# Kernel tuning notes

Hardware: AMD Instinct MI355X
Metric: run time of the kernel (lower is better)

Reference implementation:

```python
import jax, jax.numpy as jnp
import numpy as np

N = 20000      # nodes
L = 64         # seq_length
E = 64         # emb_size
V = 30000      # vocab_size
HG = 128       # gnn_hidden_size
HT = 128       # text_hidden_size
NE = 640000    # edges
EPS = 1e-12


def _normalize(x):
    # F.normalize(x, p=2, dim=1) on [N, E, L]
    n = jnp.sqrt(jnp.sum(x * x, axis=1, keepdims=True))
    return x / jnp.maximum(n, EPS)


def gcn_conv(x, W, b, src_idx, dst_idx, n_nodes):
    # PyG GCNConv: add self-loops, symmetric normalization D^-1/2 (A+I) D^-1/2 (X W) + b
    h = x @ W                                            # [N, out]
    deg = jnp.zeros((n_nodes,), h.dtype).at[dst_idx].add(1.0) + 1.0  # incl. self-loop
    dinv = jax.lax.rsqrt(deg)
    norm = dinv[src_idx] * dinv[dst_idx]                 # [NE]
    msg = h[src_idx] * norm[:, None]                     # gather + scale
    out = jnp.zeros_like(h).at[dst_idx].add(msg)         # scatter-add to targets
    out = out + h * (dinv * dinv)[:, None]               # self-loop term
    return out + b


def setup_inputs() -> dict:
    key = jax.random.key(0)
    ks = jax.random.split(key, 12)
    rn = lambda k, shape: jax.random.normal(k, shape, jnp.float32) * 0.02
    return {
        "src": jax.random.randint(ks[0], (N, L), 0, V),
        "seg": jax.random.randint(ks[1], (N, L), 0, 3),
        "edge_index": jax.random.randint(ks[2], (2, NE), 0, N),
        "src_emb": rn(ks[3], (V, E)),
        "seg_emb": rn(ks[4], (3, E)),
        "w": jnp.ones((L,), jnp.float32),
        "Wq1": rn(ks[5], (E, HT)), "bq1": jnp.zeros((HT,), jnp.float32),
        "Wq2": rn(ks[6], (HT, E)), "bq2": jnp.zeros((E,), jnp.float32),
        "Wg1": rn(ks[7], (E, HG)), "bg1": jnp.zeros((HG,), jnp.float32),
        "Wg2": rn(ks[8], (HG, E)), "bg2": jnp.zeros((E,), jnp.float32),
        "Wl": rn(ks[9], (E, E)),   "bl": jnp.zeros((E,), jnp.float32),
    }


def reference(src, seg, edge_index, src_emb, seg_emb, w, Wq1, bq1, Wq2, bq2,
              Wg1, bg1, Wg2, bg2, Wl, bl):
    # --- LiteratureEmbedding ---
    se = src_emb[src]                 # [N, L, E]
    ge = seg_emb[seg]                 # [N, L, E]
    sv = se.reshape(-1, E, L)         # raw view (matches torch .view, not transpose)
    gv = ge.reshape(-1, E, L)
    f = (_normalize(w * sv) + _normalize(gv)).sum(-1)   # [N, E]
    # --- query MLP ---
    x = jax.nn.relu(f @ Wq1 + bq1) @ Wq2 + bq2
    # --- two GCN layers ---
    si, di = edge_index[0], edge_index[1]
    x = jax.nn.relu(gcn_conv(x, Wg1, bg1, si, di, N))
    x = jax.nn.relu(gcn_conv(x, Wg2, bg2, si, di, N))
    # --- output linear (dropout is identity in eval) ---
    return x @ Wl + bl
```

## Files before the change

### kernel.cpp

```cpp
#include <hip/hip_runtime.h>

#if defined(__has_builtin)
#if __has_builtin(__builtin_amdgcn_readlane)
#define READLANE(v, l) __builtin_amdgcn_readlane((v), (l))
#else
#define READLANE(v, l) __shfl((v), (l))
#endif
#else
#define READLANE(v, l) __shfl((v), (l))
#endif
__device__ __forceinline__ float readlane_f(float v, int l) {
    return __uint_as_float(READLANE(__float_as_uint(v), l));
}

__device__ __forceinline__ unsigned short f2bf(float x) {
    unsigned u = __float_as_uint(x);
    u += 0x7FFFu + ((u >> 16) & 1u);
    return (unsigned short)(u >> 16);
}

#define CAPLOG 8

__global__ __launch_bounds__(256) void prep0_k(
    const float* __restrict__ src_emb, unsigned short* __restrict__ sbf, int ve,
    const int* __restrict__ si, const int* __restrict__ di,
    int* __restrict__ cursor, int* __restrict__ edge_off, int ne, int eB)
{
    const int b = blockIdx.x, t = threadIdx.x;
    if (b < eB) {
        int i = b * 256 + t;
        if (i < ne) {
            int d = di[i];
            int pos = atomicAdd(cursor + d, 1);
            edge_off[((long)d << CAPLOG) + pos] = si[i] << 7;
        }
        return;
    }
    int i = ((b - eB) * 256 + t) * 4;
    if (i + 3 < ve) {
        float4 v = *(const float4*)&src_emb[i];
        ushort4 u;
        u.x = f2bf(v.x); u.y = f2bf(v.y); u.z = f2bf(v.z); u.w = f2bf(v.w);
        *(ushort4*)&sbf[i] = u;
    } else {
        for (; i < ve; ++i) sbf[i] = f2bf(src_emb[i]);
    }
}

__global__ __launch_bounds__(256) void prep1_k(
    const int* __restrict__ src, const int* __restrict__ seg,
    const unsigned short* __restrict__ sbf, const float* __restrict__ seg_emb,
    const float* __restrict__ wvec, float* __restrict__ f, int nN)
{
    __shared__ float scr[4][16 * 66];
    const int t = threadIdx.x;
    const int wid = t >> 6, q = t & 63;
    const long n = (long)blockIdx.x * 4 + wid;
    if (n >= nN) return;
    const int grp = q >> 4, c = q & 15;

    const int off = src[n * 64 + q] << 7;
    const int sg  = seg[n * 64 + q];
    const float e0 = seg_emb[q], e1 = seg_emb[64 + q], e2 = seg_emb[128 + q];
    const char* base = (const char*)sbf;

    uint2 dreg[16];
    #pragma unroll
    for (int i = 0; i < 16; ++i) {
        int ro = __shfl(off, i * 4 + grp);
        dreg[i] = *(const uint2*)(base + (ro + c * 8));
    }

    float t0 = 0.f, t1 = 0.f, t2 = 0.f, t3 = 0.f;
    #pragma unroll
    for (int i = 0; i < 16; ++i) {
        float v0 = __uint_as_float(dreg[i].x << 16);
        float v1 = __uint_as_float(dreg[i].x & 0xFFFF0000u);
        float v2 = __uint_as_float(dreg[i].y << 16);
        float v3 = __uint_as_float(dreg[i].y & 0xFFFF0000u);
        t0 += v0 * v0; t1 += v1 * v1; t2 += v2 * v2; t3 += v3 * v3;
    }
    t0 += __shfl_xor(t0, 16); t0 += __shfl_xor(t0, 32);
    t1 += __shfl_xor(t1, 16); t1 += __shfl_xor(t1, 32);
    t2 += __shfl_xor(t2, 16); t2 += __shfl_xor(t2, 32);
    t3 += __shfl_xor(t3, 16); t3 += __shfl_xor(t3, 32);

    const float4 wv = *(const float4*)&wvec[c * 4];
    float4 cf;
    cf.x = wv.x / fmaxf(fabsf(wv.x) * sqrtf(t0), 1e-12f);
    cf.y = wv.y / fmaxf(fabsf(wv.y) * sqrtf(t1), 1e-12f);
    cf.z = wv.z / fmaxf(fabsf(wv.z) * sqrtf(t2), 1e-12f);
    cf.w = wv.w / fmaxf(fabsf(wv.w) * sqrtf(t3), 1e-12f);

    unsigned long long b0 = __ballot(sg == 0);
    unsigned long long b1 = __ballot(sg == 1);
    float n0 = (float)__popcll(b0), n1 = (float)__popcll(b1);
    float n2 = 64.f - n0 - n1;
    float g2 = n0 * e0 * e0 + n1 * e1 * e1 + n2 * e2 * e2;
    float rg = 1.f / fmaxf(sqrtf(g2), 1e-12f);
    float p0 = e0 * rg, p1 = e1 * rg, p2 = e2 * rg;
    #pragma unroll
    for (int m = 1; m < 64; m <<= 1) {
        p0 += __shfl_xor(p0, m);
        p1 += __shfl_xor(p1, m);
        p2 += __shfl_xor(p2, m);
    }

    float* sw = scr[wid];
    #pragma unroll
    for (int i = 0; i < 16; ++i) {
        float po = __uint_as_float(dreg[i].x << 16)          * cf.x
                 + __uint_as_float(dreg[i].x & 0xFFFF0000u)  * cf.y
                 + __uint_as_float(dreg[i].y << 16)          * cf.z
                 + __uint_as_float(dreg[i].y & 0xFFFF0000u)  * cf.w;
        sw[c * 66 + i * 4 + grp] = po;
    }
    float out = 0.f;
    #pragma unroll
    for (int c2 = 0; c2 < 16; ++c2)
        out += sw[c2 * 66 + q];

    const float dg = (sg == 0) ? p0 : ((sg == 1) ? p1 : p2);
    f[n * 64 + q] = out + dg;
}

__device__ __forceinline__ float4 csr_gather4_bf(const char* __restrict__ hb,
                                                 const int* __restrict__ eo,
                                                 int dn, int j, int zoff)
{
    const int grp = j >> 4;
    const int col = (j & 15) << 3;
    float4 a0 = make_float4(0.f, 0.f, 0.f, 0.f);
    float4 a1 = a0, a2 = a0, a3 = a0;
#define ACC(d, a)                                                        \
    { a.x += __uint_as_float((d).x << 16);                               \
      a.y += __uint_as_float((d).x & 0xFFFF0000u);                       \
      a.z += __uint_as_float((d).y << 16);                               \
      a.w += __uint_as_float((d).y & 0xFFFF0000u); }
    for (int e = 0; e < dn; e += 64) {
        const int cnt = min(dn - e, 64);
        const int eoff = (e + j < dn) ? eo[e + j] : zoff;
        int m = 0;
        for (; m + 16 <= cnt; m += 16) {
            int o0 = __shfl(eoff, m + grp);
            int o1 = __shfl(eoff, m + 4 + grp);
            int o2 = __shfl(eoff, m + 8 + grp);
            int o3 = __shfl(eoff, m + 12 + grp);
            uint2 d0 = *(const uint2*)(hb + (o0 + col));
            uint2 d1 = *(const uint2*)(hb + (o1 + col));
            uint2 d2 = *(const uint2*)(hb + (o2 + col));
            uint2 d3 = *(const uint2*)(hb + (o3 + col));
            ACC(d0, a0); ACC(d1, a1); ACC(d2, a2); ACC(d3, a3);
        }
        for (; m < cnt; m += 4) {
            int o = __shfl(eoff, m + grp);
            uint2 d = *(const uint2*)(hb + (o + col));
            ACC(d, a0);
        }
    }
#undef ACC
    a0.x += a1.x + a2.x + a3.x;
    a0.y += a1.y + a2.y + a3.y;
    a0.z += a1.z + a2.z + a3.z;
    a0.w += a1.w + a2.w + a3.w;
    a0.x += __shfl_xor(a0.x, 16); a0.x += __shfl_xor(a0.x, 32);
    a0.y += __shfl_xor(a0.y, 16); a0.y += __shfl_xor(a0.y, 32);
    a0.z += __shfl_xor(a0.z, 16); a0.z += __shfl_xor(a0.z, 32);
    a0.w += __shfl_xor(a0.w, 16); a0.w += __shfl_xor(a0.w, 32);
    return a0;
}

__device__ __forceinline__ float4 bf_row4(const char* hb, long rowoff, int col) {
    uint2 d = *(const uint2*)(hb + rowoff + col);
    float4 v;
    v.x = __uint_as_float(d.x << 16);
    v.y = __uint_as_float(d.x & 0xFFFF0000u);
    v.z = __uint_as_float(d.y << 16);
    v.w = __uint_as_float(d.y & 0xFFFF0000u);
    return v;
}

template <bool S2_BIAS>
__device__ __forceinline__ void dense_pair_body(
    float* Wh, float* F, float* H,
    const float* __restrict__ W1, const float* __restrict__ b1,
    const float* __restrict__ W2, const float* __restrict__ b2,
    const int* __restrict__ deg, unsigned short* __restrict__ out,
    int row0, int nrows, int t)
{
    for (int i = t * 4; i < 32 * 128; i += 1024)
        *(float4*)&Wh[i] = *(const float4*)&W1[i];
    __syncthreads();

    const int jg = t & 31, rslot = t >> 5;
    const int j0 = jg * 4;
    float4 acc0, acc1;
    {
        float4 b4 = *(const float4*)&b1[j0];
        acc0 = b4; acc1 = b4;
    }
    #pragma unroll 2
    for (int k = 0; k < 32; k += 4) {
        float4 w0 = *(float4*)&Wh[(k + 0) * 128 + j0];
        float4 w1 = *(float4*)&Wh[(k + 1) * 128 + j0];
        float4 w2 = *(float4*)&Wh[(k + 2) * 128 + j0];
        float4 w3 = *(float4*)&Wh[(k + 3) * 128 + j0];
        float4 fa = *(float4*)&F[rslot * 64 + k];
        float4 fb = *(float4*)&F[(rslot + 8) * 64 + k];
        acc0.x += fa.x * w0.x + fa.y * w1.x + fa.z * w2.x + fa.w * w3.x;
        acc0.y += fa.x * w0.y + fa.y * w1.y + fa.z * w2.y + fa.w * w3.y;
        acc0.z += fa.x * w0.z + fa.y * w1.z + fa.z * w2.z + fa.w * w3.z;
        acc0.w += fa.x * w0.w + fa.y * w1.w + fa.z * w2.w + fa.w * w3.w;
        acc1.x += fb.x * w0.x + fb.y * w1.x + fb.z * w2.x + fb.w * w3.x;
        acc1.y += fb.x * w0.y + fb.y * w1.y + fb.z * w2.y + fb.w * w3.y;
        acc1.z += fb.x * w0.z + fb.y * w1.z + fb.z * w2.z + fb.w * w3.z;
        acc1.w += fb.x * w0.w + fb.y * w1.w + fb.z * w2.w + fb.w * w3.w;
    }
    __syncthreads();
    for (int i = t * 4; i < 32 * 128; i += 1024)
        *(float4*)&Wh[i] = *(const float4*)&W1[32 * 128 + i];
    __syncthreads();
    #pragma unroll 2
    for (int k = 0; k < 32; k += 4) {
        float4 w0 = *(float4*)&Wh[(k + 0) * 128 + j0];
        float4 w1 = *(float4*)&Wh[(k + 1) * 128 + j0];
        float4 w2 = *(float4*)&Wh[(k + 2) * 128 + j0];
        float4 w3 = *(float4*)&Wh[(k + 3) * 128 + j0];
        float4 fa = *(float4*)&F[rslot * 64 + 32 + k];
        float4 fb = *(float4*)&F[(rslot + 8) * 64 + 32 + k];
        acc0.x += fa.x * w0.x + fa.y * w1.x + fa.z * w2.x + fa.w * w3.x;
        acc0.y += fa.x * w0.y + fa.y * w1.y + fa.z * w2.y + fa.w * w3.y;
        acc0.z += fa.x * w0.z + fa.y * w1.z + fa.z * w2.z + fa.w * w3.z;
        acc0.w += fa.x * w0.w + fa.y * w1.w + fa.z * w2.w + fa.w * w3.w;
        acc1.x += fb.x * w0.x + fb.y * w1.x + fb.z * w2.x + fb.w * w3.x;
        acc1.y += fb.x * w0.y + fb.y * w1.y + fb.z * w2.y + fb.w * w3.y;
        acc1.z += fb.x * w0.z + fb.y * w1.z + fb.z * w2.z + fb.w * w3.z;
        acc1.w += fb.x * w0.w + fb.y * w1.w + fb.z * w2.w + fb.w * w3.w;
    }
    {
        float4 v;
        v.x = fmaxf(acc0.x, 0.f); v.y = fmaxf(acc0.y, 0.f);
        v.z = fmaxf(acc0.z, 0.f); v.w = fmaxf(acc0.w, 0.f);
        *(float4*)&H[rslot * 128 + j0] = v;
        v.x = fmaxf(acc1.x, 0.f); v.y = fmaxf(acc1.y, 0.f);
        v.z = fmaxf(acc1.z, 0.f); v.w = fmaxf(acc1.w, 0.f);
        *(float4*)&H[(rslot + 8) * 128 + j0] = v;
    }
    __syncthreads();

    for (int i = t * 4; i < 64 * 64; i += 1024)
        *(float4*)&Wh[i] = *(const float4*)&W2[i];
    __syncthreads();
    const int jg2 = t & 15, r2 = t >> 4;
    const int j02 = jg2 * 4;
    float4 acc = S2_BIAS ? *(const float4*)&b2[j02]
                         : make_float4(0.f, 0.f, 0.f, 0.f);
    #pragma unroll 2
    for (int k = 0; k < 64; k += 4) {
        float4 w0 = *(float4*)&Wh[(k + 0) * 64 + j02];
        float4 w1 = *(float4*)&Wh[(k + 1) * 64 + j02];
        float4 w2 = *(float4*)&Wh[(k + 2) * 64 + j02];
        float4 w3 = *(float4*)&Wh[(k + 3) * 64 + j02];
        float4 fq = *(float4*)&H[r2 * 128 + k];
        acc.x += fq.x * w0.x + fq.y * w1.x + fq.z * w2.x + fq.w * w3.x;
        acc.y += fq.x * w0.y + fq.y * w1.y + fq.z * w2.y + fq.w * w3.y;
        acc.z += fq.x * w0.z + fq.y * w1.z + fq.z * w2.z + fq.w * w3.z;
        acc.w += fq.x * w0.w + fq.y * w1.w + fq.z * w2.w + fq.w * w3.w;
    }
    __syncthreads();
    for (int i = t * 4; i < 64 * 64; i += 1024)
        *(float4*)&Wh[i] = *(const float4*)&W2[64 * 64 + i];
    __syncthreads();
    #pragma unroll 2
    for (int k = 0; k < 64; k += 4) {
        float4 w0 = *(float4*)&Wh[(k + 0) * 64 + j02];
        float4 w1 = *(float4*)&Wh[(k + 1) * 64 + j02];
        float4 w2 = *(float4*)&Wh[(k + 2) * 64 + j02];
        float4 w3 = *(float4*)&Wh[(k + 3) * 64 + j02];
        float4 fq = *(float4*)&H[r2 * 128 + 64 + k];
        acc.x += fq.x * w0.x + fq.y * w1.x + fq.z * w2.x + fq.w * w3.x;
        acc.y += fq.x * w0.y + fq.y * w1.y + fq.z * w2.y + fq.w * w3.y;
        acc.z += fq.x * w0.z + fq.y * w1.z + fq.z * w2.z + fq.w * w3.z;
        acc.w += fq.x * w0.w + fq.y * w1.w + fq.z * w2.w + fq.w * w3.w;
    }
    const int r = row0 + r2;
    if (r < nrows) {
        float sc = rsqrtf((float)deg[r] + 1.0f);
        ushort4 v;
        v.x = f2bf(acc.x * sc); v.y = f2bf(acc.y * sc);
        v.z = f2bf(acc.z * sc); v.w = f2bf(acc.w * sc);
        *(ushort4*)&out[(long)r * 64 + j02] = v;
    }
}

template <bool S2_BIAS>
__global__ __launch_bounds__(256, 5) void fused2_k(
    const float* __restrict__ in, const float* __restrict__ W1,
    const float* __restrict__ b1, const float* __restrict__ W2,
    const float* __restrict__ b2, const int* __restrict__ deg,
    unsigned short* __restrict__ out, int nrows)
{
    __shared__ __align__(16) float Wh[32 * 128];
    __shared__ __align__(16) float F[16 * 64];
    __shared__ __align__(16) float H[16 * 128];
    const int t = threadIdx.x;
    const int row0 = blockIdx.x * 16;

    for (int i = t * 4; i < 16 * 64; i += 1024) {
        int r = i >> 6;
        float4 v = make_float4(0.f, 0.f, 0.f, 0.f);
        if (row0 + r < nrows) v = *(const float4*)&in[(long)row0 * 64 + i];
        *(float4*)&F[i] = v;
    }
    dense_pair_body<S2_BIAS>(Wh, F, H, W1, b1, W2, b2, deg, out, row0, nrows, t);
}

__global__ __launch_bounds__(256, 5) void gcnfused_k(
    const unsigned short* __restrict__ C, const int* __restrict__ deg,
    const int* __restrict__ edge_off,
    const float* __restrict__ W1, const float* __restrict__ b1,
    const float* __restrict__ W2, unsigned short* __restrict__ out,
    int nrows, int zoff)
{
    __shared__ __align__(16) float Wh[32 * 128];
    __shared__ __align__(16) float F[16 * 64];
    __shared__ __align__(16) float H[16 * 128];
    const int t = threadIdx.x;
    const int row0 = blockIdx.x * 16;
    const int wv = t >> 6, j = t & 63;
    const int col = (j & 15) << 3;

    const char* hb = (const char*)C;
    #pragma unroll
    for (int i = 0; i < 4; ++i) {
        const int r = wv * 4 + i;
        const int node = row0 + r;
        if (node < nrows) {
            float4 agg = csr_gather4_bf(hb, edge_off + ((long)node << CAPLOG),
                                        deg[node], j, zoff);
            float4 self = bf_row4(hb, (long)node << 7, col);
            float dv = rsqrtf((float)deg[node] + 1.0f);
            if ((j >> 4) == 0) {
                float4 res;
                res.x = dv * (self.x + agg.x);
                res.y = dv * (self.y + agg.y);
                res.z = dv * (self.z + agg.z);
                res.w = dv * (self.w + agg.w);
                *(float4*)&F[r * 64 + (j & 15) * 4] = res;
            }
        } else if ((j >> 4) == 0) {
            *(float4*)&F[r * 64 + (j & 15) * 4] = make_float4(0.f, 0.f, 0.f, 0.f);
        }
    }
    dense_pair_body<false>(Wh, F, H, W1, b1, W2, nullptr, deg, out, row0, nrows, t);
}

__global__ __launch_bounds__(256) void gatherout_k(
    const unsigned short* __restrict__ hp, const int* __restrict__ deg,
    const int* __restrict__ edge_off,
    const float* __restrict__ bg2, const float* __restrict__ Wl,
    const float* __restrict__ bl, float* __restrict__ out, int n, int zoff)
{
    __shared__ __align__(16) float WlL[64 * 64];
    __shared__ __align__(16) float vS[4][64];
    const int t = threadIdx.x;
    for (int i = t * 4; i < 64 * 64; i += 1024)
        *(float4*)&WlL[i] = *(const float4*)&Wl[i];
    __syncthreads();

    const int row0 = blockIdx.x * 16;
    const int wv = t >> 6, j = t & 63;
    const int col = (j & 15) << 3;
    const char* hb = (const char*)hp;
    const float blj = bl[j];
    const float4 bg4 = *(const float4*)&bg2[(j & 15) * 4];

    #pragma unroll
    for (int i = 0; i < 4; ++i) {
        const int node = row0 + wv * 4 + i;
        if (node >= n) continue;
        float4 agg = csr_gather4_bf(hb, edge_off + ((long)node << CAPLOG),
                                    deg[node], j, zoff);
        float4 self = bf_row4(hb, (long)node << 7, col);
        const float dv = rsqrtf((float)deg[node] + 1.0f);
        float4 vf;
        vf.x = fmaxf(dv * (self.x + agg.x) + bg4.x, 0.f);
        vf.y = fmaxf(dv * (self.y + agg.y) + bg4.y, 0.f);
        vf.z = fmaxf(dv * (self.z + agg.z) + bg4.z, 0.f);
        vf.w = fmaxf(dv * (self.w + agg.w) + bg4.w, 0.f);
        if ((j >> 4) == 0) *(float4*)&vS[wv][(j & 15) * 4] = vf;
        const float v = vS[wv][j];

        float o = blj;
        #pragma unroll 4
        for (int k = 0; k < 64; k += 4) {
            float vk0 = readlane_f(v, k + 0);
            float vk1 = readlane_f(v, k + 1);
            float vk2 = readlane_f(v, k + 2);
            float vk3 = readlane_f(v, k + 3);
            o += vk0 * WlL[(k + 0) * 64 + j] + vk1 * WlL[(k + 1) * 64 + j]
               + vk2 * WlL[(k + 2) * 64 + j] + vk3 * WlL[(k + 3) * 64 + j];
        }
        out[(long)node * 64 + j] = o;
    }
}

extern "C" void kernel_launch(void* const* d_in, const int* in_sizes, int n_in,
                              void* d_out, int out_size, void* d_ws, size_t ws_size,
                              hipStream_t stream) {
    const int*   src     = (const int*)  d_in[0];
    const int*   seg     = (const int*)  d_in[1];
    const int*   ei      = (const int*)  d_in[2];
    const float* src_emb = (const float*)d_in[3];
    const float* seg_emb = (const float*)d_in[4];
    const float* w       = (const float*)d_in[5];
    const float* Wq1     = (const float*)d_in[6];
    const float* bq1     = (const float*)d_in[7];
    const float* Wq2     = (const float*)d_in[8];
    const float* bq2     = (const float*)d_in[9];
    const float* Wg1     = (const float*)d_in[10];
    const float* bg1     = (const float*)d_in[11];
    const float* Wg2     = (const float*)d_in[12];
    const float* bg2     = (const float*)d_in[13];
    const float* Wl      = (const float*)d_in[14];
    const float* bl      = (const float*)d_in[15];
    float* out = (float*)d_out;

    const int N  = in_sizes[0] / 64;
    const int NE = in_sizes[2] / 2;
    const int VE = in_sizes[3];
    const int* si = ei;
    const int* di = ei + NE;

    const size_t Npad  = ((size_t)N + 3) & ~(size_t)3;
    const size_t VEpad = ((size_t)VE + 7) & ~(size_t)7;
    int* cursor   = (int*)d_ws;
    int* edge_off = cursor + Npad;
    unsigned short* sbf = (unsigned short*)(edge_off + ((size_t)N << CAPLOG));
    float* A32 = (float*)(sbf + VEpad);
    unsigned short* Cbf = (unsigned short*)(A32 + (size_t)N * 64);
    unsigned short* Abf = Cbf + (size_t)N * 64 + 64;
    const int zoff = N << 7;

    dim3 b256(256);
    const int convB = (VE + 1023) / 1024;
    const int eB    = (NE + 255) / 256;
    const int nB    = (N + 3) / 4;
    const int fB    = (N + 15) / 16;

    hipMemsetAsync(cursor, 0, Npad * sizeof(int), stream);
    hipMemsetAsync(Cbf + (size_t)N * 64, 0, 128, stream);
    hipMemsetAsync(Abf + (size_t)N * 64, 0, 128, stream);

    prep0_k<<<eB + convB, b256, 0, stream>>>(src_emb, sbf, VE,
                                             si, di, cursor, edge_off, NE, eB);

    prep1_k<<<nB, b256, 0, stream>>>(src, seg, sbf, seg_emb, w, A32, N);

    fused2_k<true><<<fB, b256, 0, stream>>>(A32, Wq1, bq1, Wq2, bq2,
                                            cursor, Cbf, N);

    gcnfused_k<<<fB, b256, 0, stream>>>(Cbf, cursor, edge_off,
                                        Wg1, bg1, Wg2, Abf, N, zoff);

    gatherout_k<<<fB, b256, 0, stream>>>(Abf, cursor, edge_off, bg2,
                                         Wl, bl, out, N, zoff);
}
```

Measured before the change: 221.8 us.

## Replace fixed-capacity per-node edge buckets with compact CSR built via prefix scan

Edges are now bucketed in two passes. A degree count runs first, then a single-block exclusive scan builds row pointers, and a second atomic pass places source offsets into a compact CSR array. The placement pass is merged into the embedding kernel launch. This replaces the padded 256-slot-per-node layout, shrinking the workspace, making gather index reads contiguous, and removing the hard degree cap. In exchange it adds a serial single-block scan launch and a second pass over the edge list with atomics.

```diff
diff --git a/kernel.cpp b/kernel.cpp
--- a/kernel.cpp
+++ b/kernel.cpp
@@ -19,21 +19,14 @@
     return (unsigned short)(u >> 16);
 }
 
-#define CAPLOG 8
-
 __global__ __launch_bounds__(256) void prep0_k(
     const float* __restrict__ src_emb, unsigned short* __restrict__ sbf, int ve,
-    const int* __restrict__ si, const int* __restrict__ di,
-    int* __restrict__ cursor, int* __restrict__ edge_off, int ne, int eB)
+    const int* __restrict__ di, int* __restrict__ cursor, int ne, int eB)
 {
     const int b = blockIdx.x, t = threadIdx.x;
     if (b < eB) {
         int i = b * 256 + t;
-        if (i < ne) {
-            int d = di[i];
-            int pos = atomicAdd(cursor + d, 1);
-            edge_off[((long)d << CAPLOG) + pos] = si[i] << 7;
-        }
+        if (i < ne) atomicAdd(cursor + di[i], 1);
         return;
     }
     int i = ((b - eB) * 256 + t) * 4;
@@ -47,15 +40,73 @@
     }
 }
 
-__global__ __launch_bounds__(256) void prep1_k(
+__global__ __launch_bounds__(1024) void scan_k(
+    const int* __restrict__ deg, int* __restrict__ rowptr,
+    int* __restrict__ pcur, int n,
+    unsigned* __restrict__ Cz, unsigned* __restrict__ Az)
+{
+    __shared__ int wsum[16];
+    const int t = threadIdx.x;
+    const int lane = t & 63, wid = t >> 6;
+    const int CH = (n + 1023) >> 10;
+    const int base = t * CH;
+
+    int s = 0;
+    for (int i = 0; i < CH; ++i) {
+        int idx = base + i;
+        s += (idx < n) ? deg[idx] : 0;
+    }
+    int x = s;
+    #pragma unroll
+    for (int d = 1; d < 64; d <<= 1) {
+        int v = __shfl_up(x, d);
+        if (lane >= d) x += v;
+    }
+    if (lane == 63) wsum[wid] = x;
+    __syncthreads();
+    if (wid == 0 && lane < 16) {
+        int v = wsum[lane];
+        int y = v;
+        #pragma unroll
+        for (int d = 1; d < 16; d <<= 1) {
+            int u = __shfl_up(y, d);
+            if (lane >= d) y += u;
+        }
+        wsum[lane] = y - v;
+    }
+    __syncthreads();
+    int run = wsum[wid] + (x - s);
+    for (int i = 0; i < CH; ++i) {
+        int idx = base + i;
+        if (idx < n) {
+            rowptr[idx] = run;
+            pcur[idx]   = run;
+            run += deg[idx];
+        }
+    }
+    if (t < 32) { Cz[t] = 0u; Az[t] = 0u; }
+}
+
+__global__ __launch_bounds__(256) void prep2_k(
+    const int* __restrict__ si, const int* __restrict__ di,
+    int* __restrict__ pcur, int* __restrict__ edge_col, int ne, int eB,
     const int* __restrict__ src, const int* __restrict__ seg,
     const unsigned short* __restrict__ sbf, const float* __restrict__ seg_emb,
     const float* __restrict__ wvec, float* __restrict__ f, int nN)
 {
+    const int t = threadIdx.x;
+    if ((int)blockIdx.x < eB) {
+        int i = blockIdx.x * 256 + t;
+        if (i < ne) {
+            int d = di[i];
+            int pos = atomicAdd(pcur + d, 1);
+            edge_col[pos] = si[i] << 7;
+        }
+        return;
+    }
     __shared__ float scr[4][16 * 66];
-    const int t = threadIdx.x;
     const int wid = t >> 6, q = t & 63;
-    const long n = (long)blockIdx.x * 4 + wid;
+    const long n = ((long)blockIdx.x - eB) * 4 + wid;
     if (n >= nN) return;
     const int grp = q >> 4, c = q & 15;
 
@@ -317,7 +368,7 @@
 
 __global__ __launch_bounds__(256, 5) void gcnfused_k(
     const unsigned short* __restrict__ C, const int* __restrict__ deg,
-    const int* __restrict__ edge_off,
+    const int* __restrict__ rowptr, const int* __restrict__ edge_col,
     const float* __restrict__ W1, const float* __restrict__ b1,
     const float* __restrict__ W2, unsigned short* __restrict__ out,
     int nrows, int zoff)
@@ -336,7 +387,7 @@
         const int r = wv * 4 + i;
         const int node = row0 + r;
         if (node < nrows) {
-            float4 agg = csr_gather4_bf(hb, edge_off + ((long)node << CAPLOG),
+            float4 agg = csr_gather4_bf(hb, edge_col + rowptr[node],
                                         deg[node], j, zoff);
             float4 self = bf_row4(hb, (long)node << 7, col);
             float dv = rsqrtf((float)deg[node] + 1.0f);
@@ -357,7 +408,7 @@
 
 __global__ __launch_bounds__(256) void gatherout_k(
     const unsigned short* __restrict__ hp, const int* __restrict__ deg,
-    const int* __restrict__ edge_off,
+    const int* __restrict__ rowptr, const int* __restrict__ edge_col,
     const float* __restrict__ bg2, const float* __restrict__ Wl,
     const float* __restrict__ bl, float* __restrict__ out, int n, int zoff)
 {
@@ -379,7 +430,7 @@
     for (int i = 0; i < 4; ++i) {
         const int node = row0 + wv * 4 + i;
         if (node >= n) continue;
-        float4 agg = csr_gather4_bf(hb, edge_off + ((long)node << CAPLOG),
+        float4 agg = csr_gather4_bf(hb, edge_col + rowptr[node],
                                     deg[node], j, zoff);
         float4 self = bf_row4(hb, (long)node << 7, col);
         const float dv = rsqrtf((float)deg[node] + 1.0f);
@@ -433,10 +484,13 @@
     const int* di = ei + NE;
 
     const size_t Npad  = ((size_t)N + 3) & ~(size_t)3;
+    const size_t NEpad = ((size_t)NE + 3) & ~(size_t)3;
     const size_t VEpad = ((size_t)VE + 7) & ~(size_t)7;
     int* cursor   = (int*)d_ws;
-    int* edge_off = cursor + Npad;
-    unsigned short* sbf = (unsigned short*)(edge_off + ((size_t)N << CAPLOG));
+    int* rowptr   = cursor + Npad;
+    int* pcur     = rowptr + Npad;
+    int* edge_col = pcur + Npad;
+    unsigned short* sbf = (unsigned short*)(edge_col + NEpad);
     float* A32 = (float*)(sbf + VEpad);
     unsigned short* Cbf = (unsigned short*)(A32 + (size_t)N * 64);
     unsigned short* Abf = Cbf + (size_t)N * 64 + 64;
@@ -449,20 +503,23 @@
     const int fB    = (N + 15) / 16;
 
     hipMemsetAsync(cursor, 0, Npad * sizeof(int), stream);
-    hipMemsetAsync(Cbf + (size_t)N * 64, 0, 128, stream);
-    hipMemsetAsync(Abf + (size_t)N * 64, 0, 128, stream);
 
     prep0_k<<<eB + convB, b256, 0, stream>>>(src_emb, sbf, VE,
-                                             si, di, cursor, edge_off, NE, eB);
-
-    prep1_k<<<nB, b256, 0, stream>>>(src, seg, sbf, seg_emb, w, A32, N);
+                                             di, cursor, NE, eB);
+
+    scan_k<<<1, 1024, 0, stream>>>(cursor, rowptr, pcur, N,
+                                   (unsigned*)(Cbf + (size_t)N * 64),
+                                   (unsigned*)(Abf + (size_t)N * 64));
+
+    prep2_k<<<eB + nB, b256, 0, stream>>>(si, di, pcur, edge_col, NE, eB,
+                                          src, seg, sbf, seg_emb, w, A32, N);
 
     fused2_k<true><<<fB, b256, 0, stream>>>(A32, Wq1, bq1, Wq2, bq2,
                                             cursor, Cbf, N);
 
-    gcnfused_k<<<fB, b256, 0, stream>>>(Cbf, cursor, edge_off,
+    gcnfused_k<<<fB, b256, 0, stream>>>(Cbf, cursor, rowptr, edge_col,
                                         Wg1, bg1, Wg2, Abf, N, zoff);
 
-    gatherout_k<<<fB, b256, 0, stream>>>(Abf, cursor, edge_off, bg2,
+    gatherout_k<<<fB, b256, 0, stream>>>(Abf, cursor, rowptr, edge_col, bg2,
                                          Wl, bl, out, N, zoff);
 }
```

Result: slower. 288.0 us (+29.8%).
